# Optimization experiments

Measured on AMD Instinct MI355X. Metric: run time of the kernel, lower is better.

Reference implementation:

```python
import jax, jax.numpy as jnp
import numpy as np

N = 100_000      # nodes
E = 1_600_000    # directed edges
D_IN, D_H, D_OUT = 128, 128, 1


def setup_inputs() -> dict:
    key = jax.random.key(0)
    ks = jax.random.split(key, 6)
    x = jax.random.normal(ks[0], (N, D_IN), dtype=jnp.float32)
    edge_index = jax.random.randint(ks[1], (2, E), 0, N, dtype=jnp.int32)
    # GCNConv params (glorot-ish scale)
    W1 = jax.random.normal(ks[2], (D_IN, D_H), dtype=jnp.float32) / np.sqrt(D_IN)
    b1 = jnp.zeros((D_H,), dtype=jnp.float32)
    W2 = jax.random.normal(ks[3], (D_H, D_OUT), dtype=jnp.float32) / np.sqrt(D_H)
    b2 = jnp.zeros((D_OUT,), dtype=jnp.float32)
    return {"x": x, "edge_index": edge_index, "W1": W1, "b1": b1, "W2": W2, "b2": b2}


def _gcn_layer(x, src, dst, norm, W, b):
    # PyG GCNConv: linear transform, then sym-normalized neighbor sum (self-loops included in src/dst)
    h = x @ W                                  # [N, d_out]
    msg = h[src] * norm[:, None]               # [E+N, d_out] gather + scale
    out = jax.ops.segment_sum(msg, dst, num_segments=N)  # scatter-add
    return out + b


def reference(x, edge_index, W1, b1, W2, b2):
    loops = jnp.arange(N, dtype=edge_index.dtype)
    src = jnp.concatenate([edge_index[0], loops])  # [E+N]
    dst = jnp.concatenate([edge_index[1], loops])
    # symmetric normalization D^{-1/2} (A+I) D^{-1/2}
    deg = jax.ops.segment_sum(jnp.ones_like(dst, dtype=x.dtype), dst, num_segments=N)
    dis = jnp.where(deg > 0, jax.lax.rsqrt(deg), 0.0)
    norm = dis[src] * dis[dst]
    h = jax.nn.relu(_gcn_layer(x, src, dst, norm, W1, b1))
    return _gcn_layer(h, src, dst, norm, W2, b2)
```

## Files before the change

### kernel.cpp

```cpp
#include <hip/hip_runtime.h>
#include <hip/hip_fp16.h>

#define D 128
#define BSHIFT 9
#define MAXB 512
#define CHUNK 8192
#define CAP 12288
#define GP 8
#define OSTR 144

#define QS   (6.5f / 127.f)
#define QSI  (127.f / 6.5f)
#define WSC  (QS / 8192.f)

typedef _Float16 f16x8 __attribute__((ext_vector_type(8)));
typedef float f32x4 __attribute__((ext_vector_type(4)));

__global__ void setup_k(const float* __restrict__ W1, _Float16* __restrict__ w1t,
                        int* __restrict__ bcur, unsigned char* __restrict__ h1s8,
                        float* __restrict__ g, float* __restrict__ dis, int N) {
    int idx = blockIdx.x * 256 + threadIdx.x;
    int k = idx >> 7, n = idx & 127;
    w1t[n * 128 + k] = (_Float16)W1[idx];
    if (blockIdx.x == 0) {
        bcur[threadIdx.x] = 0;
        bcur[threadIdx.x + 256] = 0;
        if (threadIdx.x < 8) {
            int4 z = {0, 0, 0, 0};
            ((int4*)(h1s8 + (size_t)N * 128))[threadIdx.x] = z;
        }
        if (threadIdx.x == 0) { g[N] = 0.f; dis[N] = 0.f; }
    }
}

__global__ __launch_bounds__(512) void bin_k(const int* __restrict__ src,
                                             const int* __restrict__ dst,
                                             int* __restrict__ bcur,
                                             unsigned int* __restrict__ pairs, int E) {
    __shared__ int h[MAXB];
    __shared__ int cur[MAXB];
    if (threadIdx.x < MAXB) h[threadIdx.x] = 0;
    __syncthreads();
    const int base = blockIdx.x * CHUNK;
    int s_[16], d_[16];
    int n = 0;
#pragma unroll
    for (int u = 0; u < 16; ++u) {
        int e = base + u * 512 + threadIdx.x;
        if (e < E) {
            s_[u] = src[e];
            d_[u] = dst[e];
            atomicAdd(&h[d_[u] >> BSHIFT], 1);
            n = u + 1;
        }
    }
    __syncthreads();
    if (threadIdx.x < MAXB) {
        int i = threadIdx.x;
        cur[i] = h[i] ? (i * CAP + atomicAdd(&bcur[i], h[i])) : 0;
    }
    __syncthreads();
#pragma unroll
    for (int u = 0; u < 16; ++u) {
        if (u < n) {
            int b = d_[u] >> BSHIFT;
            int pos = atomicAdd(&cur[b], 1);
            if (pos - b * CAP < CAP)
                pairs[pos] = ((unsigned int)(d_[u] & ((1 << BSHIFT) - 1)) << 23) |
                             (unsigned int)s_[u];
        }
    }
}

__global__ __launch_bounds__(512) void csr_k(const unsigned int* __restrict__ pairs,
                                             const int* __restrict__ bcur,
                                             int* __restrict__ offs,
                                             int* __restrict__ deg,
                                             float* __restrict__ dis,
                                             int* __restrict__ edge_src, int N) {
    __shared__ int hist[512];
    __shared__ int scan[512];
    __shared__ int cur[512];
    __shared__ int buf[CAP];
    const int b = blockIdx.x;
    const int t = threadIdx.x;
    const int vb = b << BSHIFT;
    const int ebeg = b * CAP;
    int cnt = bcur[b]; cnt = cnt < CAP ? cnt : CAP;
    const int eend = ebeg + cnt;

    hist[t] = 0;
    for (int j = t; j < CAP; j += 512) buf[j] = N;
    __syncthreads();
    for (int e = ebeg + t; e < eend; e += 512)
        atomicAdd(&hist[pairs[e] >> 23], 1);
    __syncthreads();

    const int c = hist[t];
    const int p8 = (c + 7) & ~7;
    scan[t] = p8;
    __syncthreads();
    for (int o = 1; o < 512; o <<= 1) {
        int a = (t >= o) ? scan[t - o] : 0;
        __syncthreads();
        scan[t] += a;
        __syncthreads();
    }

    {
        int v = vb + t;
        if (v < N) {
            int base_rel = scan[t] - p8;
            offs[v] = ebeg + base_rel;
            deg[v] = c;
            cur[t] = base_rel;
            dis[v] = rsqrtf((float)(c + 1));
        }
    }
    __syncthreads();

    for (int e = ebeg + t; e < eend; e += 512) {
        unsigned int p = pairs[e];
        int pos = atomicAdd(&cur[p >> 23], 1);
        buf[pos] = (int)(p & 0x7FFFFFu);
    }
    __syncthreads();

    for (int j = t; j < (CAP >> 2); j += 512)
        ((int4*)(edge_src + ebeg))[j] = ((const int4*)buf)[j];
}

__global__ __launch_bounds__(256) void pack_k(int* __restrict__ edge_src,
                                              const float* __restrict__ dis,
                                              int total4) {
    int j = blockIdx.x * 256 + threadIdx.x;
    if (j >= total4) return;
    int4 e = ((const int4*)edge_src)[j];
    int4 o;
    o.x = ((int)rintf(dis[e.x] * 8192.f) << 17) | e.x;
    o.y = ((int)rintf(dis[e.y] * 8192.f) << 17) | e.y;
    o.z = ((int)rintf(dis[e.z] * 8192.f) << 17) | e.z;
    o.w = ((int)rintf(dis[e.w] * 8192.f) << 17) | e.w;
    ((int4*)edge_src)[j] = o;
}


__global__ __launch_bounds__(256) void gemm_k(const float* __restrict__ x,
                                              const _Float16* __restrict__ w1t,
                                              unsigned char* __restrict__ h1s8, int N) {
    __shared__ _Float16 xs[128][128 + GP];
    __shared__ _Float16 ws[128][128 + GP];

    const int tid = threadIdx.x;
    const int row0 = blockIdx.x * 128;

#pragma unroll
    for (int u = 0; u < 16; ++u) {
        int f = u * 256 + tid;
        int r = f >> 5, c4 = f & 31;
        int rg = row0 + r; rg = rg < N ? rg : N - 1;
        float4 v = ((const float4*)(x + (size_t)rg * D))[c4];
        union { _Float16 h[4]; uint2 u2; } tmp;
        tmp.h[0] = (_Float16)v.x; tmp.h[1] = (_Float16)v.y;
        tmp.h[2] = (_Float16)v.z; tmp.h[3] = (_Float16)v.w;
        *(uint2*)&xs[r][c4 * 4] = tmp.u2;
    }
#pragma unroll
    for (int u = 0; u < 8; ++u) {
        int f = u * 256 + tid;
        int r = f >> 4, c8 = f & 15;
        int4 v = ((const int4*)(w1t + r * 128))[c8];
        *(int4*)&ws[r][c8 * 8] = v;
    }
    __syncthreads();

    const int wave = tid >> 6, lane = tid & 63;
    const int qr = lane & 15;
    const int quad = lane >> 4;
    const int m0 = wave * 32;

    f32x4 acc[2][8] = {};
#pragma unroll
    for (int kt = 0; kt < 4; ++kt) {
        const int kk = kt * 32 + quad * 8;
        f16x8 a0 = *(const f16x8*)&xs[m0 + qr][kk];
        f16x8 a1 = *(const f16x8*)&xs[m0 + 16 + qr][kk];
#pragma unroll
        for (int n = 0; n < 8; ++n) {
            f16x8 b = *(const f16x8*)&ws[n * 16 + qr][kk];
            acc[0][n] = __builtin_amdgcn_mfma_f32_16x16x32_f16(a0, b, acc[0][n], 0, 0, 0);
            acc[1][n] = __builtin_amdgcn_mfma_f32_16x16x32_f16(a1, b, acc[1][n], 0, 0, 0);
        }
    }

    __syncthreads();
    unsigned char* os = (unsigned char*)&ws[0][0];
#pragma unroll
    for (int mt = 0; mt < 2; ++mt)
#pragma unroll
        for (int n = 0; n < 8; ++n)
#pragma unroll
            for (int r = 0; r < 4; ++r) {
                int row = m0 + mt * 16 + quad * 4 + r;
                float qf = fminf(fmaxf(acc[mt][n][r] * QSI, -127.f), 127.f);
                int q = (int)rintf(qf);
                os[row * OSTR + n * 16 + qr] = (unsigned char)(q & 0xFF);
            }
    __syncthreads();

#pragma unroll
    for (int u = 0; u < 4; ++u) {
        int f = u * 256 + tid;
        int r = f >> 3, c16 = f & 7;
        int rg = row0 + r;
        if (rg < N)
            ((int4*)(h1s8 + (size_t)rg * 128))[c16] = *(const int4*)(os + r * OSTR + c16 * 16);
    }
}


__device__ __forceinline__ void accw(float* aq, int Wd, float wt) {
    aq[0] = fmaf(wt, (float)((Wd << 24) >> 24), aq[0]);
    aq[1] = fmaf(wt, (float)((Wd << 16) >> 24), aq[1]);
    aq[2] = fmaf(wt, (float)((Wd <<  8) >> 24), aq[2]);
    aq[3] = fmaf(wt, (float)( Wd        >> 24), aq[3]);
}
__device__ __forceinline__ void accr(float* a, const int4& rr, float wt) {
    accw(a +  0, rr.x, wt);
    accw(a +  4, rr.y, wt);
    accw(a +  8, rr.z, wt);
    accw(a + 12, rr.w, wt);
}

__global__ __launch_bounds__(256) void agg1_k(const unsigned char* __restrict__ h1s8,
                                              const int* __restrict__ edge_src,
                                              const int* __restrict__ offs,
                                              const int* __restrict__ deg,
                                              const float* __restrict__ dis,
                                              const float* __restrict__ b1,
                                              const float* __restrict__ W2,
                                              float* __restrict__ g, int N) {
    const int c = threadIdx.x & 7;
    const int v = blockIdx.x * 32 + (threadIdx.x >> 3);
    if (v >= N) return;

    const float dv = dis[v];
    float a[16] = {};
    {
        int4 sv = *(const int4*)(h1s8 + (size_t)v * 128 + c * 16);
        accr(a, sv, dv * QS);
    }

    const int beg = offs[v];
    const int p8 = (deg[v] + 7) & ~7;
    const int4* ip = (const int4*)(edge_src + beg);
    int4 s0 = ip[0], s1 = ip[1];

    for (int i = 0; i < p8; i += 8) {
        int4 n0 = ip[2], n1 = ip[3];
        int i0 = s0.x & 0x1FFFF, i1 = s0.y & 0x1FFFF;
        int i2 = s0.z & 0x1FFFF, i3 = s0.w & 0x1FFFF;
        int i4 = s1.x & 0x1FFFF, i5 = s1.y & 0x1FFFF;
        int i6 = s1.z & 0x1FFFF, i7 = s1.w & 0x1FFFF;
        float w0 = (float)((unsigned)s0.x >> 17) * WSC;
        float w1 = (float)((unsigned)s0.y >> 17) * WSC;
        float w2 = (float)((unsigned)s0.z >> 17) * WSC;
        float w3 = (float)((unsigned)s0.w >> 17) * WSC;
        float w4 = (float)((unsigned)s1.x >> 17) * WSC;
        float w5 = (float)((unsigned)s1.y >> 17) * WSC;
        float w6 = (float)((unsigned)s1.z >> 17) * WSC;
        float w7 = (float)((unsigned)s1.w >> 17) * WSC;
        int4 r0 = *(const int4*)(h1s8 + (size_t)i0 * 128 + c * 16);
        int4 r1 = *(const int4*)(h1s8 + (size_t)i1 * 128 + c * 16);
        int4 r2 = *(const int4*)(h1s8 + (size_t)i2 * 128 + c * 16);
        int4 r3 = *(const int4*)(h1s8 + (size_t)i3 * 128 + c * 16);
        int4 r4 = *(const int4*)(h1s8 + (size_t)i4 * 128 + c * 16);
        int4 r5 = *(const int4*)(h1s8 + (size_t)i5 * 128 + c * 16);
        int4 r6 = *(const int4*)(h1s8 + (size_t)i6 * 128 + c * 16);
        int4 r7 = *(const int4*)(h1s8 + (size_t)i7 * 128 + c * 16);
        accr(a, r0, w0); accr(a, r1, w1); accr(a, r2, w2); accr(a, r3, w3);
        accr(a, r4, w4); accr(a, r5, w5); accr(a, r6, w6); accr(a, r7, w7);
        s0 = n0; s1 = n1; ip += 2;
    }

    float p = 0.f;
#pragma unroll
    for (int q4 = 0; q4 < 4; ++q4) {
        float4 bb = ((const float4*)b1)[c * 4 + q4];
        float4 ww = ((const float4*)W2)[c * 4 + q4];
        p += fmaxf(fmaf(dv, a[q4 * 4 + 0], bb.x), 0.f) * ww.x
           + fmaxf(fmaf(dv, a[q4 * 4 + 1], bb.y), 0.f) * ww.y
           + fmaxf(fmaf(dv, a[q4 * 4 + 2], bb.z), 0.f) * ww.z
           + fmaxf(fmaf(dv, a[q4 * 4 + 3], bb.w), 0.f) * ww.w;
    }
#pragma unroll
    for (int o = 4; o >= 1; o >>= 1) p += __shfl_xor(p, o, 64);
    if (c == 0) g[v] = dv * p;
}


__global__ void agg2_k(const float* __restrict__ g, const int* __restrict__ edge_src,
                       const int* __restrict__ offs, const int* __restrict__ deg,
                       const float* __restrict__ dis, const float* __restrict__ b2,
                       float* __restrict__ out, int N) {
    int v = blockIdx.x * 256 + threadIdx.x;
    if (v >= N) return;
    float acc = g[v];
    const int beg = offs[v];
    const int p8 = (deg[v] + 7) & ~7;
    const int4* ip = (const int4*)(edge_src + beg);
    for (int i = 0; i < p8; i += 4) {
        int4 s = ip[i >> 2];
        acc += (g[s.x & 0x1FFFF] + g[s.y & 0x1FFFF])
             + (g[s.z & 0x1FFFF] + g[s.w & 0x1FFFF]);
    }
    out[v] = fmaf(dis[v], acc, b2[0]);
}


extern "C" void kernel_launch(void* const* d_in, const int* in_sizes, int n_in,
                              void* d_out, int out_size, void* d_ws, size_t ws_size,
                              hipStream_t stream) {
    const float* x  = (const float*)d_in[0];
    const int*   ei = (const int*)d_in[1];
    const float* W1 = (const float*)d_in[2];
    const float* b1 = (const float*)d_in[3];
    const float* W2 = (const float*)d_in[4];
    const float* b2 = (const float*)d_in[5];
    float* out = (float*)d_out;

    const int N = in_sizes[0] / D;
    const int E = in_sizes[1] / 2;
    const int* srcp = ei;
    const int* dstp = ei + E;
    const int nbuck = (N + (1 << BSHIFT) - 1) >> BSHIFT;

    char* p = (char*)d_ws;
    auto alloc = [&](size_t bytes) {
        void* q = (void*)p;
        p += (bytes + 255) & ~(size_t)255;
        return q;
    };
    unsigned char* h1s8     = (unsigned char*)alloc((size_t)(N + 1) * 128);
    float*         g        = (float*)alloc((size_t)(N + 1) * sizeof(float));
    float*         dis      = (float*)alloc((size_t)(N + 1) * sizeof(float));
    int*           offs     = (int*)alloc((size_t)N * sizeof(int));
    int*           deg      = (int*)alloc((size_t)N * sizeof(int));
    int*           edge_src = (int*)alloc((size_t)nbuck * CAP * sizeof(int));
    unsigned int*  pairs    = (unsigned int*)alloc((size_t)nbuck * CAP * sizeof(unsigned int));
    _Float16*      w1t      = (_Float16*)alloc((size_t)D * D * sizeof(_Float16));
    int*           bcur     = (int*)alloc(MAXB * sizeof(int));

    const int nb = (N + 255) / 256;
    const int total4 = nbuck * (CAP / 4);

    setup_k<<<(D * D) / 256, 256, 0, stream>>>(W1, w1t, bcur, h1s8, g, dis, N);
    bin_k<<<(E + CHUNK - 1) / CHUNK, 512, 0, stream>>>(srcp, dstp, bcur, pairs, E);
    csr_k<<<nbuck, 512, 0, stream>>>(pairs, bcur, offs, deg, dis, edge_src, N);
    pack_k<<<(total4 + 255) / 256, 256, 0, stream>>>(edge_src, dis, total4);
    gemm_k<<<(N + 127) / 128, 256, 0, stream>>>(x, w1t, h1s8, N);
    agg1_k<<<(N + 31) / 32, 256, 0, stream>>>(h1s8, edge_src, offs, deg, dis, b1, W2, g, N);
    agg2_k<<<nb, 256, 0, stream>>>(g, edge_src, offs, deg, dis, b2, out, N);
}
```

Before: 186.0 us.

## Replace bucketed CSR build with global atomic degree count, scan, and scatter

Replaces the two-pass bucket binning (bin_k, csr_k, pack_k) with a global-atomic degree histogram, a two-level prefix scan, and a direct atomic scatter into a compact CSR that packs the quantised source normalisation as it writes. This removes the fixed-capacity bucket arrays, the intermediate pairs buffer and the separate pack pass. It also drops the silent truncation of buckets that overflow CAP. In exchange it relies on global atomics into random destinations and scattered writes, with more kernel launches, and the edge order within each row is no longer deterministic.

New measurement: 362.5 us. 1.95x slower.

```diff
diff --git a/kernel.cpp b/kernel.cpp
--- a/kernel.cpp
+++ b/kernel.cpp
@@ -2,10 +2,6 @@
 #include <hip/hip_fp16.h>
 
 #define D 128
-#define BSHIFT 9
-#define MAXB 512
-#define CHUNK 8192
-#define CAP 12288
 #define GP 8
 #define OSTR 144
 
@@ -17,131 +13,116 @@
 typedef float f32x4 __attribute__((ext_vector_type(4)));
 
 __global__ void setup_k(const float* __restrict__ W1, _Float16* __restrict__ w1t,
-                        int* __restrict__ bcur, unsigned char* __restrict__ h1s8,
+                        int* __restrict__ deg, unsigned char* __restrict__ h1s8,
                         float* __restrict__ g, float* __restrict__ dis, int N) {
     int idx = blockIdx.x * 256 + threadIdx.x;
-    int k = idx >> 7, n = idx & 127;
-    w1t[n * 128 + k] = (_Float16)W1[idx];
-    if (blockIdx.x == 0) {
-        bcur[threadIdx.x] = 0;
-        bcur[threadIdx.x + 256] = 0;
-        if (threadIdx.x < 8) {
-            int4 z = {0, 0, 0, 0};
-            ((int4*)(h1s8 + (size_t)N * 128))[threadIdx.x] = z;
-        }
-        if (threadIdx.x == 0) { g[N] = 0.f; dis[N] = 0.f; }
-    }
-}
-
-__global__ __launch_bounds__(512) void bin_k(const int* __restrict__ src,
-                                             const int* __restrict__ dst,
-                                             int* __restrict__ bcur,
-                                             unsigned int* __restrict__ pairs, int E) {
-    __shared__ int h[MAXB];
-    __shared__ int cur[MAXB];
-    if (threadIdx.x < MAXB) h[threadIdx.x] = 0;
-    __syncthreads();
-    const int base = blockIdx.x * CHUNK;
-    int s_[16], d_[16];
-    int n = 0;
-#pragma unroll
-    for (int u = 0; u < 16; ++u) {
-        int e = base + u * 512 + threadIdx.x;
-        if (e < E) {
-            s_[u] = src[e];
-            d_[u] = dst[e];
-            atomicAdd(&h[d_[u] >> BSHIFT], 1);
-            n = u + 1;
-        }
-    }
-    __syncthreads();
-    if (threadIdx.x < MAXB) {
-        int i = threadIdx.x;
-        cur[i] = h[i] ? (i * CAP + atomicAdd(&bcur[i], h[i])) : 0;
-    }
-    __syncthreads();
-#pragma unroll
-    for (int u = 0; u < 16; ++u) {
-        if (u < n) {
-            int b = d_[u] >> BSHIFT;
-            int pos = atomicAdd(&cur[b], 1);
-            if (pos - b * CAP < CAP)
-                pairs[pos] = ((unsigned int)(d_[u] & ((1 << BSHIFT) - 1)) << 23) |
-                             (unsigned int)s_[u];
-        }
-    }
-}
-
-__global__ __launch_bounds__(512) void csr_k(const unsigned int* __restrict__ pairs,
-                                             const int* __restrict__ bcur,
+    if (idx < D * D) {
+        int k = idx >> 7, n = idx & 127;
+        w1t[n * 128 + k] = (_Float16)W1[idx];
+    }
+    if (idx < N) deg[idx] = 0;
+    if (idx < 8) {
+        int4 z = {0, 0, 0, 0};
+        ((int4*)(h1s8 + (size_t)N * 128))[idx] = z;
+    }
+    if (idx == 0) { g[N] = 0.f; dis[N] = 0.f; }
+}
+
+__global__ __launch_bounds__(256) void deg_k(const int* __restrict__ dst,
+                                             int* __restrict__ deg, int E) {
+    int j = (blockIdx.x * 256 + threadIdx.x) * 4;
+    if (j + 3 < E) {
+        int4 d = *(const int4*)(dst + j);
+        atomicAdd(&deg[d.x], 1); atomicAdd(&deg[d.y], 1);
+        atomicAdd(&deg[d.z], 1); atomicAdd(&deg[d.w], 1);
+    } else {
+        for (; j < E; ++j) atomicAdd(&deg[dst[j]], 1);
+    }
+}
+
+__global__ __launch_bounds__(512) void scanA_k(const int* __restrict__ deg,
+                                               int* __restrict__ loffs,
+                                               int* __restrict__ bsum, int N) {
+    __shared__ int sc[512];
+    const int t = threadIdx.x;
+    const int v = blockIdx.x * 512 + t;
+    int c = (v < N) ? deg[v] : 0;
+    int p8 = (c + 7) & ~7;
+    sc[t] = p8;
+    __syncthreads();
+    for (int o = 1; o < 512; o <<= 1) {
+        int a = (t >= o) ? sc[t - o] : 0;
+        __syncthreads();
+        sc[t] += a;
+        __syncthreads();
+    }
+    if (v < N) loffs[v] = sc[t] - p8;
+    if (t == 511) bsum[blockIdx.x] = sc[511];
+}
+
+__global__ __launch_bounds__(256) void scanB_k(int* __restrict__ bsum, int NB) {
+    __shared__ int sc[256];
+    const int t = threadIdx.x;
+    int x = (t < NB) ? bsum[t] : 0;
+    sc[t] = x;
+    __syncthreads();
+    for (int o = 1; o < 256; o <<= 1) {
+        int a = (t >= o) ? sc[t - o] : 0;
+        __syncthreads();
+        sc[t] += a;
+        __syncthreads();
+    }
+    if (t < NB) bsum[t] = sc[t] - x;
+}
+
+__global__ __launch_bounds__(256) void fin_k(const int* __restrict__ deg,
+                                             const int* __restrict__ loffs,
+                                             const int* __restrict__ bsum,
                                              int* __restrict__ offs,
-                                             int* __restrict__ deg,
+                                             int* __restrict__ cur,
                                              float* __restrict__ dis,
                                              int* __restrict__ edge_src, int N) {
-    __shared__ int hist[512];
-    __shared__ int scan[512];
-    __shared__ int cur[512];
-    __shared__ int buf[CAP];
-    const int b = blockIdx.x;
-    const int t = threadIdx.x;
-    const int vb = b << BSHIFT;
-    const int ebeg = b * CAP;
-    int cnt = bcur[b]; cnt = cnt < CAP ? cnt : CAP;
-    const int eend = ebeg + cnt;
-
-    hist[t] = 0;
-    for (int j = t; j < CAP; j += 512) buf[j] = N;
-    __syncthreads();
-    for (int e = ebeg + t; e < eend; e += 512)
-        atomicAdd(&hist[pairs[e] >> 23], 1);
-    __syncthreads();
-
-    const int c = hist[t];
-    const int p8 = (c + 7) & ~7;
-    scan[t] = p8;
-    __syncthreads();
-    for (int o = 1; o < 512; o <<= 1) {
-        int a = (t >= o) ? scan[t - o] : 0;
-        __syncthreads();
-        scan[t] += a;
-        __syncthreads();
-    }
-
-    {
-        int v = vb + t;
-        if (v < N) {
-            int base_rel = scan[t] - p8;
-            offs[v] = ebeg + base_rel;
-            deg[v] = c;
-            cur[t] = base_rel;
-            dis[v] = rsqrtf((float)(c + 1));
+    int v = blockIdx.x * 256 + threadIdx.x;
+    if (v >= N) return;
+    int c = deg[v];
+    int p8 = (c + 7) & ~7;
+    int off = bsum[v >> 9] + loffs[v];
+    offs[v] = off;
+    cur[v] = off;
+    dis[v] = rsqrtf((float)(c + 1));
+    for (int i = c; i < p8; ++i) edge_src[off + i] = N;
+}
+
+__global__ __launch_bounds__(256) void scat_k(const int* __restrict__ src,
+                                              const int* __restrict__ dst,
+                                              const float* __restrict__ dis,
+                                              int* __restrict__ cur,
+                                              int* __restrict__ edge_src, int E) {
+    int j = (blockIdx.x * 256 + threadIdx.x) * 4;
+    if (j >= E) return;
+    if (j + 3 < E) {
+        int4 s = *(const int4*)(src + j);
+        int4 d = *(const int4*)(dst + j);
+        int q0 = (int)rintf(dis[s.x] * 8192.f);
+        int q1 = (int)rintf(dis[s.y] * 8192.f);
+        int q2 = (int)rintf(dis[s.z] * 8192.f);
+        int q3 = (int)rintf(dis[s.w] * 8192.f);
+        int p0 = atomicAdd(&cur[d.x], 1);
+        int p1 = atomicAdd(&cur[d.y], 1);
+        int p2 = atomicAdd(&cur[d.z], 1);
+        int p3 = atomicAdd(&cur[d.w], 1);
+        edge_src[p0] = (q0 << 17) | s.x;
+        edge_src[p1] = (q1 << 17) | s.y;
+        edge_src[p2] = (q2 << 17) | s.z;
+        edge_src[p3] = (q3 << 17) | s.w;
+    } else {
+        for (; j < E; ++j) {
+            int s = src[j], d = dst[j];
+            int q = (int)rintf(dis[s] * 8192.f);
+            int p = atomicAdd(&cur[d], 1);
+            edge_src[p] = (q << 17) | s;
         }
     }
-    __syncthreads();
-
-    for (int e = ebeg + t; e < eend; e += 512) {
-        unsigned int p = pairs[e];
-        int pos = atomicAdd(&cur[p >> 23], 1);
-        buf[pos] = (int)(p & 0x7FFFFFu);
-    }
-    __syncthreads();
-
-    for (int j = t; j < (CAP >> 2); j += 512)
-        ((int4*)(edge_src + ebeg))[j] = ((const int4*)buf)[j];
-}
-
-__global__ __launch_bounds__(256) void pack_k(int* __restrict__ edge_src,
-                                              const float* __restrict__ dis,
-                                              int total4) {
-    int j = blockIdx.x * 256 + threadIdx.x;
-    if (j >= total4) return;
-    int4 e = ((const int4*)edge_src)[j];
-    int4 o;
-    o.x = ((int)rintf(dis[e.x] * 8192.f) << 17) | e.x;
-    o.y = ((int)rintf(dis[e.y] * 8192.f) << 17) | e.y;
-    o.z = ((int)rintf(dis[e.z] * 8192.f) << 17) | e.z;
-    o.w = ((int)rintf(dis[e.w] * 8192.f) << 17) | e.w;
-    ((int4*)edge_src)[j] = o;
 }
 
 
@@ -333,7 +314,6 @@
     const int E = in_sizes[1] / 2;
     const int* srcp = ei;
     const int* dstp = ei + E;
-    const int nbuck = (N + (1 << BSHIFT) - 1) >> BSHIFT;
 
     char* p = (char*)d_ws;
     auto alloc = [&](size_t bytes) {
@@ -346,18 +326,22 @@
     float*         dis      = (float*)alloc((size_t)(N + 1) * sizeof(float));
     int*           offs     = (int*)alloc((size_t)N * sizeof(int));
     int*           deg      = (int*)alloc((size_t)N * sizeof(int));
-    int*           edge_src = (int*)alloc((size_t)nbuck * CAP * sizeof(int));
-    unsigned int*  pairs    = (unsigned int*)alloc((size_t)nbuck * CAP * sizeof(unsigned int));
+    int*           cur      = (int*)alloc((size_t)N * sizeof(int));
+    int*           loffs    = (int*)alloc((size_t)N * sizeof(int));
+    int*           bsum     = (int*)alloc(256 * sizeof(int));
+    int*           edge_src = (int*)alloc(((size_t)E + 7 * (size_t)N + 64) * sizeof(int));
     _Float16*      w1t      = (_Float16*)alloc((size_t)D * D * sizeof(_Float16));
-    int*           bcur     = (int*)alloc(MAXB * sizeof(int));
-
-    const int nb = (N + 255) / 256;
-    const int total4 = nbuck * (CAP / 4);
-
-    setup_k<<<(D * D) / 256, 256, 0, stream>>>(W1, w1t, bcur, h1s8, g, dis, N);
-    bin_k<<<(E + CHUNK - 1) / CHUNK, 512, 0, stream>>>(srcp, dstp, bcur, pairs, E);
-    csr_k<<<nbuck, 512, 0, stream>>>(pairs, bcur, offs, deg, dis, edge_src, N);
-    pack_k<<<(total4 + 255) / 256, 256, 0, stream>>>(edge_src, dis, total4);
+
+    const int nb   = (N + 255) / 256;
+    const int nbE4 = (E / 4 + 255) / 256;
+    const int NB   = (N + 511) / 512;
+
+    setup_k<<<nb, 256, 0, stream>>>(W1, w1t, deg, h1s8, g, dis, N);
+    deg_k<<<nbE4, 256, 0, stream>>>(dstp, deg, E);
+    scanA_k<<<NB, 512, 0, stream>>>(deg, loffs, bsum, N);
+    scanB_k<<<1, 256, 0, stream>>>(bsum, NB);
+    fin_k<<<nb, 256, 0, stream>>>(deg, loffs, bsum, offs, cur, dis, edge_src, N);
+    scat_k<<<nbE4, 256, 0, stream>>>(srcp, dstp, dis, cur, edge_src, E);
     gemm_k<<<(N + 127) / 128, 256, 0, stream>>>(x, w1t, h1s8, N);
     agg1_k<<<(N + 31) / 32, 256, 0, stream>>>(h1s8, edge_src, offs, deg, dis, b1, W2, g, N);
     agg2_k<<<nb, 256, 0, stream>>>(g, edge_src, offs, deg, dis, b2, out, N);
```

## Split CSR build into degree pass and scatter pass, fuse dis packing into scatter

Applied to the files above, without the earlier changes.

The CSR construction is split into two kernels. The first computes histogram, offsets, degree and dis. The second scatters sources and packs the quantized dis weight into each edge entry directly, which removes the separate pack_k pass over the whole edge buffer. agg2 now software-prefetches the next two int4 index vectors while summing the current eight neighbors, and edge_src is padded so that prefetch stays in bounds. The cost is reading pairs twice, plus one extra launch and a random dis gather inside the scatter.

Result: no change. 182.7 us (-1.8%).

```diff
diff --git a/kernel.cpp b/kernel.cpp
--- a/kernel.cpp
+++ b/kernel.cpp
@@ -72,14 +72,50 @@
     }
 }
 
-__global__ __launch_bounds__(512) void csr_k(const unsigned int* __restrict__ pairs,
-                                             const int* __restrict__ bcur,
-                                             int* __restrict__ offs,
-                                             int* __restrict__ deg,
-                                             float* __restrict__ dis,
-                                             int* __restrict__ edge_src, int N) {
+__global__ __launch_bounds__(512) void csrA_k(const unsigned int* __restrict__ pairs,
+                                              const int* __restrict__ bcur,
+                                              int* __restrict__ offs,
+                                              int* __restrict__ deg,
+                                              float* __restrict__ dis, int N) {
     __shared__ int hist[512];
     __shared__ int scan[512];
+    const int b = blockIdx.x;
+    const int t = threadIdx.x;
+    const int vb = b << BSHIFT;
+    const int ebeg = b * CAP;
+    int cnt = bcur[b]; cnt = cnt < CAP ? cnt : CAP;
+    const int eend = ebeg + cnt;
+
+    hist[t] = 0;
+    __syncthreads();
+    for (int e = ebeg + t; e < eend; e += 512)
+        atomicAdd(&hist[pairs[e] >> 23], 1);
+    __syncthreads();
+
+    const int c = hist[t];
+    const int p8 = (c + 7) & ~7;
+    scan[t] = p8;
+    __syncthreads();
+    for (int o = 1; o < 512; o <<= 1) {
+        int a = (t >= o) ? scan[t - o] : 0;
+        __syncthreads();
+        scan[t] += a;
+        __syncthreads();
+    }
+
+    int v = vb + t;
+    if (v < N) {
+        offs[v] = ebeg + scan[t] - p8;
+        deg[v] = c;
+        dis[v] = rsqrtf((float)(c + 1));
+    }
+}
+
+__global__ __launch_bounds__(512) void csrB_k(const unsigned int* __restrict__ pairs,
+                                              const int* __restrict__ bcur,
+                                              const int* __restrict__ offs,
+                                              const float* __restrict__ dis,
+                                              int* __restrict__ edge_src, int N) {
     __shared__ int cur[512];
     __shared__ int buf[CAP];
     const int b = blockIdx.x;
@@ -89,59 +125,24 @@
     int cnt = bcur[b]; cnt = cnt < CAP ? cnt : CAP;
     const int eend = ebeg + cnt;
 
-    hist[t] = 0;
     for (int j = t; j < CAP; j += 512) buf[j] = N;
-    __syncthreads();
-    for (int e = ebeg + t; e < eend; e += 512)
-        atomicAdd(&hist[pairs[e] >> 23], 1);
-    __syncthreads();
-
-    const int c = hist[t];
-    const int p8 = (c + 7) & ~7;
-    scan[t] = p8;
-    __syncthreads();
-    for (int o = 1; o < 512; o <<= 1) {
-        int a = (t >= o) ? scan[t - o] : 0;
-        __syncthreads();
-        scan[t] += a;
-        __syncthreads();
-    }
-
     {
         int v = vb + t;
-        if (v < N) {
-            int base_rel = scan[t] - p8;
-            offs[v] = ebeg + base_rel;
-            deg[v] = c;
-            cur[t] = base_rel;
-            dis[v] = rsqrtf((float)(c + 1));
-        }
+        cur[t] = (v < N) ? (offs[v] - ebeg) : 0;
     }
     __syncthreads();
 
     for (int e = ebeg + t; e < eend; e += 512) {
         unsigned int p = pairs[e];
+        int s = (int)(p & 0x7FFFFFu);
+        int q = (int)rintf(dis[s] * 8192.f);
         int pos = atomicAdd(&cur[p >> 23], 1);
-        buf[pos] = (int)(p & 0x7FFFFFu);
+        buf[pos] = (q << 17) | s;
     }
     __syncthreads();
 
     for (int j = t; j < (CAP >> 2); j += 512)
         ((int4*)(edge_src + ebeg))[j] = ((const int4*)buf)[j];
-}
-
-__global__ __launch_bounds__(256) void pack_k(int* __restrict__ edge_src,
-                                              const float* __restrict__ dis,
-                                              int total4) {
-    int j = blockIdx.x * 256 + threadIdx.x;
-    if (j >= total4) return;
-    int4 e = ((const int4*)edge_src)[j];
-    int4 o;
-    o.x = ((int)rintf(dis[e.x] * 8192.f) << 17) | e.x;
-    o.y = ((int)rintf(dis[e.y] * 8192.f) << 17) | e.y;
-    o.z = ((int)rintf(dis[e.z] * 8192.f) << 17) | e.z;
-    o.w = ((int)rintf(dis[e.w] * 8192.f) << 17) | e.w;
-    ((int4*)edge_src)[j] = o;
 }
 
 
@@ -309,10 +310,14 @@
     const int beg = offs[v];
     const int p8 = (deg[v] + 7) & ~7;
     const int4* ip = (const int4*)(edge_src + beg);
-    for (int i = 0; i < p8; i += 4) {
-        int4 s = ip[i >> 2];
-        acc += (g[s.x & 0x1FFFF] + g[s.y & 0x1FFFF])
-             + (g[s.z & 0x1FFFF] + g[s.w & 0x1FFFF]);
+    int4 s0 = ip[0], s1 = ip[1];
+    for (int i = 0; i < p8; i += 8) {
+        int4 n0 = ip[2], n1 = ip[3];
+        acc += (g[s0.x & 0x1FFFF] + g[s0.y & 0x1FFFF])
+             + (g[s0.z & 0x1FFFF] + g[s0.w & 0x1FFFF])
+             + (g[s1.x & 0x1FFFF] + g[s1.y & 0x1FFFF])
+             + (g[s1.z & 0x1FFFF] + g[s1.w & 0x1FFFF]);
+        s0 = n0; s1 = n1; ip += 2;
     }
     out[v] = fmaf(dis[v], acc, b2[0]);
 }
@@ -346,18 +351,17 @@
     float*         dis      = (float*)alloc((size_t)(N + 1) * sizeof(float));
     int*           offs     = (int*)alloc((size_t)N * sizeof(int));
     int*           deg      = (int*)alloc((size_t)N * sizeof(int));
-    int*           edge_src = (int*)alloc((size_t)nbuck * CAP * sizeof(int));
+    int*           edge_src = (int*)alloc(((size_t)nbuck * CAP + 64) * sizeof(int));
     unsigned int*  pairs    = (unsigned int*)alloc((size_t)nbuck * CAP * sizeof(unsigned int));
     _Float16*      w1t      = (_Float16*)alloc((size_t)D * D * sizeof(_Float16));
     int*           bcur     = (int*)alloc(MAXB * sizeof(int));
 
     const int nb = (N + 255) / 256;
-    const int total4 = nbuck * (CAP / 4);
 
     setup_k<<<(D * D) / 256, 256, 0, stream>>>(W1, w1t, bcur, h1s8, g, dis, N);
     bin_k<<<(E + CHUNK - 1) / CHUNK, 512, 0, stream>>>(srcp, dstp, bcur, pairs, E);
-    csr_k<<<nbuck, 512, 0, stream>>>(pairs, bcur, offs, deg, dis, edge_src, N);
-    pack_k<<<(total4 + 255) / 256, 256, 0, stream>>>(edge_src, dis, total4);
+    csrA_k<<<nbuck, 512, 0, stream>>>(pairs, bcur, offs, deg, dis, N);
+    csrB_k<<<nbuck, 512, 0, stream>>>(pairs, bcur, offs, dis, edge_src, N);
     gemm_k<<<(N + 127) / 128, 256, 0, stream>>>(x, w1t, h1s8, N);
     agg1_k<<<(N + 31) / 32, 256, 0, stream>>>(h1s8, edge_src, offs, deg, dis, b1, W2, g, N);
     agg2_k<<<nb, 256, 0, stream>>>(g, edge_src, offs, deg, dis, b2, out, N);
```
